# Optimization experiments

Hardware: AMD Instinct MI355X
Metric: run time of the kernel (lower is better)

## Reference

```python
import jax, jax.numpy as jnp
import numpy as np

PI = float(np.pi)

def _quantize_angle(theta):
    deg = theta * (180.0 / PI)
    deg = jnp.where(deg < 0, deg + 180.0, deg)
    q = jnp.round(deg / 45.0) * 45.0
    # 180 is treated the same as 0 in the original branch (theta==0 or theta==180)
    return jnp.where(q == 180.0, 0.0, q)

def setup_inputs() -> dict:
    key = jax.random.key(0)
    k1, k2 = jax.random.split(key)
    H, W = 4096, 4096
    img = jax.random.uniform(k1, (1, 1, H, W), dtype=jnp.float32)
    theta = jax.random.normal(k2, (1, 1, H, W), dtype=jnp.float32)  # radians
    return {"img": img, "theta": theta}

def reference(img, theta):
    q = _quantize_angle(theta)

    # value of neighbor at (x+dx, y+dy); borders are masked out afterwards so
    # roll wrap-around never affects the result (interior pixels only).
    def nbr(dx, dy):
        return jnp.roll(img, shift=(-dx, -dy), axis=(2, 3))

    def local_max(dx, dy):
        return (img >= nbr(dx, dy)) & (img >= nbr(-dx, -dy))

    m0 = local_max(0, 1)     # theta == 0 / 180: compare (x, y+-1)
    m45 = local_max(1, 1)    # theta == 45:      compare (x+-1, y+-1)
    m90 = local_max(1, 0)    # theta == 90:      compare (x+-1, y)
    m135 = local_max(1, -1)  # theta == 135:     compare (x+1,y-1),(x-1,y+1)

    mask = jnp.where(q == 0.0, m0,
           jnp.where(q == 45.0, m45,
           jnp.where(q == 90.0, m90, m135)))

    H, W = img.shape[2], img.shape[3]
    interior = jnp.zeros((H, W), dtype=bool).at[1:-1, 1:-1].set(True)
    return jnp.where(mask & interior, img, jnp.zeros_like(img))
```

## Files before the change

kernel.cpp:

```cpp
#include <hip/hip_runtime.h>
#include <math.h>

#define IMG_H 4096
#define IMG_W 4096

__global__ __launch_bounds__(256) void nms_kernel(const float* __restrict__ img,
                                                  const float* __restrict__ theta,
                                                  float* __restrict__ out) {
    const int tid = blockIdx.x * blockDim.x + threadIdx.x;
    const int x  = tid >> 10;
    const int y4 = (tid & 1023) << 2;

    const long long base = (long long)x * IMG_W + y4;

    const int xu = (x > 0)        ? x - 1 : 0;
    const int xd = (x < IMG_H - 1) ? x + 1 : IMG_H - 1;

    const float* rowc = img + (long long)x  * IMG_W;
    const float* rowu = img + (long long)xu * IMG_W;
    const float* rowd = img + (long long)xd * IMG_W;

    const float4 c = *(const float4*)(rowc + y4);
    const float4 u = *(const float4*)(rowu + y4);
    const float4 d = *(const float4*)(rowd + y4);
    const float4 th = *(const float4*)(theta + base);

    const int yl = (y4 > 0)           ? y4 - 1 : 0;
    const int yr = (y4 + 4 < IMG_W)   ? y4 + 4 : IMG_W - 1;
    const float cl = rowc[yl], cr = rowc[yr];
    const float ul = rowu[yl], ur = rowu[yr];
    const float dl = rowd[yl], dr = rowd[yr];

    const float cv[6] = {cl, c.x, c.y, c.z, c.w, cr};
    const float uv[6] = {ul, u.x, u.y, u.z, u.w, ur};
    const float dv[6] = {dl, d.x, d.y, d.z, d.w, dr};
    const float tv[4] = {th.x, th.y, th.z, th.w};

    float ov[4];
    const bool row_interior = (x > 0) && (x < IMG_H - 1);

    #pragma unroll
    for (int i = 0; i < 4; ++i) {
        const float v = cv[i + 1];

        float deg = tv[i] * 57.29577951308232f;
        if (deg < 0.0f) deg += 180.0f;
        float q = rintf(deg / 45.0f) * 45.0f;
        if (q == 180.0f) q = 0.0f;

        float a, b;
        if (q == 0.0f) {
            a = cv[i + 2]; b = cv[i];
        } else if (q == 45.0f) {
            a = dv[i + 2]; b = uv[i];
        } else if (q == 90.0f) {
            a = dv[i + 1]; b = uv[i + 1];
        } else {
            a = dv[i]; b = uv[i + 2];
        }

        const int y = y4 + i;
        const bool interior = row_interior && (y > 0) && (y < IMG_W - 1);
        const bool mask = (v >= a) && (v >= b);
        ov[i] = (mask && interior) ? v : 0.0f;
    }

    float4 o;
    o.x = ov[0]; o.y = ov[1]; o.z = ov[2]; o.w = ov[3];
    *(float4*)(out + base) = o;
}

extern "C" void kernel_launch(void* const* d_in, const int* in_sizes, int n_in,
                              void* d_out, int out_size, void* d_ws, size_t ws_size,
                              hipStream_t stream) {
    const float* img   = (const float*)d_in[0];
    const float* theta = (const float*)d_in[1];
    float* out = (float*)d_out;

    const int total_threads = IMG_H * (IMG_W / 4);
    const int block = 256;
    const int grid = total_threads / block;
    nms_kernel<<<grid, block, 0, stream>>>(img, theta, out);
}
```

Baseline: 175.3 us.

## Process eight rows per thread with a sliding three-row register window

Each thread now handles a column strip of eight consecutive rows and keeps the up, center and down rows in registers, loading only one new row per output row. The intent is to cut the redundant global and cache reads of the neighbouring rows, which were each loaded three times before. In exchange there are fewer threads (one eighth as many), so less parallelism is available to hide memory latency, and register use goes up.

New measurement: 175.6 us. No clear change (+0.2%).

```diff
diff --git a/kernel.cpp b/kernel.cpp
--- a/kernel.cpp
+++ b/kernel.cpp
@@ -3,71 +3,83 @@
 
 #define IMG_H 4096
 #define IMG_W 4096
+#define ROWS_PER_THREAD 8
 
 __global__ __launch_bounds__(256) void nms_kernel(const float* __restrict__ img,
                                                   const float* __restrict__ theta,
                                                   float* __restrict__ out) {
     const int tid = blockIdx.x * blockDim.x + threadIdx.x;
-    const int x  = tid >> 10;
-    const int y4 = (tid & 1023) << 2;
+    const int g  = tid >> 10;
+    const int qc = tid & 1023;
+    const int y4 = qc << 2;
+    const int x0 = g * ROWS_PER_THREAD;
 
-    const long long base = (long long)x * IMG_W + y4;
+    const int yl = (y4 > 0)         ? y4 - 1 : 0;
+    const int yr = (y4 + 4 < IMG_W) ? y4 + 4 : IMG_W - 1;
 
-    const int xu = (x > 0)        ? x - 1 : 0;
-    const int xd = (x < IMG_H - 1) ? x + 1 : IMG_H - 1;
+    auto load_row = [&](int x, float4& v, float& el, float& er) {
+        const float* row = img + (long long)x * IMG_W;
+        v  = *(const float4*)(row + y4);
+        el = row[yl];
+        er = row[yr];
+    };
 
-    const float* rowc = img + (long long)x  * IMG_W;
-    const float* rowu = img + (long long)xu * IMG_W;
-    const float* rowd = img + (long long)xd * IMG_W;
+    float4 u, c, d;
+    float ul, ur, cl, cr, dl, dr;
 
-    const float4 c = *(const float4*)(rowc + y4);
-    const float4 u = *(const float4*)(rowu + y4);
-    const float4 d = *(const float4*)(rowd + y4);
-    const float4 th = *(const float4*)(theta + base);
-
-    const int yl = (y4 > 0)           ? y4 - 1 : 0;
-    const int yr = (y4 + 4 < IMG_W)   ? y4 + 4 : IMG_W - 1;
-    const float cl = rowc[yl], cr = rowc[yr];
-    const float ul = rowu[yl], ur = rowu[yr];
-    const float dl = rowd[yl], dr = rowd[yr];
-
-    const float cv[6] = {cl, c.x, c.y, c.z, c.w, cr};
-    const float uv[6] = {ul, u.x, u.y, u.z, u.w, ur};
-    const float dv[6] = {dl, d.x, d.y, d.z, d.w, dr};
-    const float tv[4] = {th.x, th.y, th.z, th.w};
-
-    float ov[4];
-    const bool row_interior = (x > 0) && (x < IMG_H - 1);
+    const int xu0 = (x0 > 0) ? x0 - 1 : 0;
+    load_row(xu0, u, ul, ur);
+    load_row(x0,  c, cl, cr);
 
     #pragma unroll
-    for (int i = 0; i < 4; ++i) {
-        const float v = cv[i + 1];
+    for (int i = 0; i < ROWS_PER_THREAD; ++i) {
+        const int x  = x0 + i;
+        const int xd = (x < IMG_H - 1) ? x + 1 : IMG_H - 1;
+        load_row(xd, d, dl, dr);
 
-        float deg = tv[i] * 57.29577951308232f;
-        if (deg < 0.0f) deg += 180.0f;
-        float q = rintf(deg / 45.0f) * 45.0f;
-        if (q == 180.0f) q = 0.0f;
+        const long long base = (long long)x * IMG_W + y4;
+        const float4 th = *(const float4*)(theta + base);
 
-        float a, b;
-        if (q == 0.0f) {
-            a = cv[i + 2]; b = cv[i];
-        } else if (q == 45.0f) {
-            a = dv[i + 2]; b = uv[i];
-        } else if (q == 90.0f) {
-            a = dv[i + 1]; b = uv[i + 1];
-        } else {
-            a = dv[i]; b = uv[i + 2];
+        const float cv[6] = {cl, c.x, c.y, c.z, c.w, cr};
+        const float uv[6] = {ul, u.x, u.y, u.z, u.w, ur};
+        const float dv[6] = {dl, d.x, d.y, d.z, d.w, dr};
+        const float tv[4] = {th.x, th.y, th.z, th.w};
+
+        const bool row_interior = (x > 0) && (x < IMG_H - 1);
+        float ov[4];
+
+        #pragma unroll
+        for (int j = 0; j < 4; ++j) {
+            const float v = cv[j + 1];
+
+            float deg = tv[j] * 57.29577951308232f;
+            if (deg < 0.0f) deg += 180.0f;
+            float q = rintf(deg / 45.0f) * 45.0f;
+            if (q == 180.0f) q = 0.0f;
+
+            float a, b;
+            if (q == 0.0f) {
+                a = cv[j + 2]; b = cv[j];
+            } else if (q == 45.0f) {
+                a = dv[j + 2]; b = uv[j];
+            } else if (q == 90.0f) {
+                a = dv[j + 1]; b = uv[j + 1];
+            } else {
+                a = dv[j]; b = uv[j + 2];
+            }
+
+            const int y = y4 + j;
+            const bool interior = row_interior && (y > 0) && (y < IMG_W - 1);
+            ov[j] = ((v >= a) && (v >= b) && interior) ? v : 0.0f;
         }
 
-        const int y = y4 + i;
-        const bool interior = row_interior && (y > 0) && (y < IMG_W - 1);
-        const bool mask = (v >= a) && (v >= b);
-        ov[i] = (mask && interior) ? v : 0.0f;
+        float4 o;
+        o.x = ov[0]; o.y = ov[1]; o.z = ov[2]; o.w = ov[3];
+        *(float4*)(out + base) = o;
+
+        u = c; ul = cl; ur = cr;
+        c = d; cl = dl; cr = dr;
     }
-
-    float4 o;
-    o.x = ov[0]; o.y = ov[1]; o.z = ov[2]; o.w = ov[3];
-    *(float4*)(out + base) = o;
 }
 
 extern "C" void kernel_launch(void* const* d_in, const int* in_sizes, int n_in,
@@ -77,7 +89,7 @@
     const float* theta = (const float*)d_in[1];
     float* out = (float*)d_out;
 
-    const int total_threads = IMG_H * (IMG_W / 4);
+    const int total_threads = (IMG_H / ROWS_PER_THREAD) * (IMG_W / 4);
     const int block = 256;
     const int grid = total_threads / block;
     nms_kernel<<<grid, block, 0, stream>>>(img, theta, out);
```
